# Optimization experiments

Hardware: AMD Instinct MI355X
Metric: run time of the kernel (lower is better)

## Reference

```python
import jax, jax.numpy as jnp
import numpy as np
from jax import lax

B, C, H, W = 8, 128, 256, 256
OUT_CH = 64
IN_CH = C * 9  # 1152: module's in_channels = 9 * image channels (unfold with 3x3 kernel)


def setup_inputs() -> dict:
    key = jax.random.key(0)
    k1, k2, k3 = jax.random.split(key, 3)
    x = jax.random.normal(k1, (B, C, H, W), dtype=jnp.float32)
    style = jax.random.normal(k2, (B, IN_CH), dtype=jnp.float32)
    # learned parameter: torch.randn(out_channels, in_channels, 1, 1) -> store as (out, in)
    weight = jax.random.normal(k3, (OUT_CH, IN_CH), dtype=jnp.float32)
    return {"x": x, "style": style, "weight": weight}


def reference(x, style, weight):
    b, c, h, w = x.shape
    out_ch, in_ch = weight.shape  # in_ch == c * 9
    # unfold column ordering is (c, kh, kw), so the flattened weight is exactly a
    # 3x3 conv kernel: (out, c*9) -> (out, c, 3, 3)
    w33 = weight.reshape(out_ch, c, 3, 3)
    # style.view(B,1,in_ch,1,1) * weight -> per-sample modulated 3x3 kernels
    w_mod = style.reshape(b, 1, c, 3, 3) * w33[None]  # (B, out, c, 3, 3)

    def conv_one(xi, wi):
        # xi: (c, h, w), wi: (out, c, 3, 3); SAME padding matches padding=(1,1)
        return lax.conv_general_dilated(
            xi[None], wi, window_strides=(1, 1), padding="SAME",
            dimension_numbers=("NCHW", "OIHW", "NCHW"))[0]

    out = jax.vmap(conv_one)(x, w_mod)  # (B, out, h, w)
    return out
```

## Files before the change

kernel.cpp:

```cpp
#include <hip/hip_runtime.h>
#include <hip/hip_bf16.h>

#define BATCH 8
#define CIN   128
#define HH    256
#define WW    256
#define OUTC  64
#define INCH  1152
#define HW    (HH*WW)

typedef __attribute__((ext_vector_type(8))) short short8;
typedef __attribute__((ext_vector_type(4))) float f32x4;

__device__ __forceinline__ unsigned short bf16r(float f) {
    unsigned u = __builtin_bit_cast(unsigned, f);
    u += 0x7fffu + ((u >> 16) & 1u);
    return (unsigned short)(u >> 16);
}

__global__ void __launch_bounds__(256) wmod_kernel(const float* __restrict__ weight,
                                                   const float* __restrict__ style,
                                                   unsigned short* __restrict__ wmod) {
    int i = blockIdx.x * 256 + threadIdx.x;
    if (i >= BATCH * 9 * OUTC * CIN) return;
    int c    = i & (CIN - 1);
    int rest = i >> 7;
    int o    = rest & (OUTC - 1);
    int bt   = rest >> 6;
    int tap  = bt % 9;
    int b    = bt / 9;
    int k    = c * 9 + tap;
    float v = weight[o * INCH + k] * style[b * INCH + k];
    wmod[i] = bf16r(v);
}

template <bool GW>
__global__ void __launch_bounds__(256, 4) conv_kernel(
    const float* __restrict__ x,
    const unsigned short* __restrict__ wmod,
    const float* __restrict__ weight,
    const float* __restrict__ style,
    float* __restrict__ out)
{
    __shared__ __align__(16) unsigned short xs_sm[170 * 64];

    const int tid = threadIdx.x;
    const int bx  = blockIdx.x;
    const int b   = blockIdx.y;
    const int h0  = (bx >> 3) * 8;
    const int w0  = (bx & 7) * 32;

    const int wv  = tid >> 6;
    const int l15 = tid & 15;
    const int kg  = (tid >> 4) & 3;

    int prow[4], pcol[4];
#pragma unroll
    for (int ni = 0; ni < 4; ++ni) {
        int p = wv * 64 + ni * 16 + l15;
        prow[ni] = p >> 5;
        pcol[ni] = p & 31;
    }

    f32x4 acc[4][4];
#pragma unroll
    for (int mi = 0; mi < 4; ++mi)
#pragma unroll
        for (int ni = 0; ni < 4; ++ni) acc[mi][ni] = (f32x4){0.f, 0.f, 0.f, 0.f};

    for (int chunk = 0; chunk < 4; ++chunk) {
        if (chunk) __syncthreads();

        const float* xb = x + ((size_t)(b * CIN + chunk * 32)) * HW;
        for (int t = tid; t < 1360; t += 256) {
            int cg  = t / 340;
            int s   = t - cg * 340;
            int r   = s / 34;
            int col = s - r * 34;
            int h = h0 - 1 + r, w = w0 - 1 + col;
            bool ok = ((unsigned)h < HH) && ((unsigned)w < WW);
            int off = h * WW + w;
            const float* xc = xb + (size_t)(cg * 8) * HW;
            short8 sv;
#pragma unroll
            for (int j = 0; j < 8; ++j) {
                float f = ok ? xc[(size_t)j * HW + off] : 0.f;
                sv[j] = (short)bf16r(f);
            }
            int q = s >> 1;
            int g = (((s & 1) << 2) | cg) ^ (q & 7);
            *(short8*)&xs_sm[q * 64 + g * 8] = sv;
        }
        __syncthreads();

        const unsigned short* wmb = wmod + ((size_t)(b * 9) * OUTC) * CIN + chunk * 32;
#pragma unroll
        for (int tap = 0; tap < 9; ++tap) {
            const int kh = tap / 3, kw = tap % 3;

            short8 A[4];
            if (GW) {
                const unsigned short* wt = wmb + (size_t)tap * OUTC * CIN;
#pragma unroll
                for (int mi = 0; mi < 4; ++mi)
                    A[mi] = *(const short8*)(wt + (mi * 16 + l15) * CIN + kg * 8);
            } else {
#pragma unroll
                for (int mi = 0; mi < 4; ++mi) {
                    int o = mi * 16 + l15;
#pragma unroll
                    for (int j = 0; j < 8; ++j) {
                        int c = chunk * 32 + kg * 8 + j;
                        int k = c * 9 + tap;
                        A[mi][j] = (short)bf16r(weight[o * INCH + k] *
                                                style[b * INCH + k]);
                    }
                }
            }

            short8 Bv[4];
#pragma unroll
            for (int ni = 0; ni < 4; ++ni) {
                int s = (prow[ni] + kh) * 34 + pcol[ni] + kw;
                int q = s >> 1;
                int g = (((s & 1) << 2) | kg) ^ (q & 7);
                Bv[ni] = *(const short8*)&xs_sm[q * 64 + g * 8];
            }
#pragma unroll
            for (int mi = 0; mi < 4; ++mi)
#pragma unroll
                for (int ni = 0; ni < 4; ++ni)
                    acc[mi][ni] = __builtin_amdgcn_mfma_f32_16x16x32_bf16(
                        A[mi], Bv[ni], acc[mi][ni], 0, 0, 0);
        }
    }

    float* op = out + ((size_t)b * OUTC) * HW;
#pragma unroll
    for (int mi = 0; mi < 4; ++mi) {
#pragma unroll
        for (int ni = 0; ni < 4; ++ni) {
            int p = wv * 64 + ni * 16 + l15;
            int h = h0 + (p >> 5), w = w0 + (p & 31);
#pragma unroll
            for (int r = 0; r < 4; ++r) {
                int o = mi * 16 + kg * 4 + r;
                op[(size_t)o * HW + h * WW + w] = acc[mi][ni][r];
            }
        }
    }
}

extern "C" void kernel_launch(void* const* d_in, const int* in_sizes, int n_in,
                              void* d_out, int out_size, void* d_ws, size_t ws_size,
                              hipStream_t stream) {
    const float* x      = (const float*)d_in[0];
    const float* style  = (const float*)d_in[1];
    const float* weight = (const float*)d_in[2];
    float* out = (float*)d_out;

    const size_t wmod_bytes = (size_t)BATCH * 9 * OUTC * CIN * sizeof(unsigned short);
    if (ws_size >= wmod_bytes) {
        int total = BATCH * 9 * OUTC * CIN;
        wmod_kernel<<<(total + 255) / 256, 256, 0, stream>>>(weight, style,
                                                             (unsigned short*)d_ws);
        conv_kernel<true><<<dim3(256, BATCH), 256, 0, stream>>>(
            x, (const unsigned short*)d_ws, nullptr, nullptr, out);
    } else {
        conv_kernel<false><<<dim3(256, BATCH), 256, 0, stream>>>(
            x, nullptr, weight, style, out);
    }
}
```

Measured before the change: 248.7 us.

## Double-buffer LDS input tiles to overlap staging with MFMA compute

Doubles the shared-memory input tile and restructures the channel-chunk loop so the next chunk is loaded and converted to bf16 while the current chunk runs its MFMAs, with one barrier per chunk instead of two. Per-thread staging offsets, bounds masks and swizzled LDS addresses are precomputed once rather than recomputed with divisions every chunk. The larger LDS footprint and extra registers lower the occupancy bound from 4 to 3 blocks per CU, which may reduce latency hiding elsewhere.

After: 306.7 us. 23.4% more time.

```diff
diff --git a/kernel.cpp b/kernel.cpp
--- a/kernel.cpp
+++ b/kernel.cpp
@@ -35,14 +35,14 @@
 }
 
 template <bool GW>
-__global__ void __launch_bounds__(256, 4) conv_kernel(
+__global__ void __launch_bounds__(256, 3) conv_kernel(
     const float* __restrict__ x,
     const unsigned short* __restrict__ wmod,
     const float* __restrict__ weight,
     const float* __restrict__ style,
     float* __restrict__ out)
 {
-    __shared__ __align__(16) unsigned short xs_sm[170 * 64];
+    __shared__ __align__(16) unsigned short xs_sm[2][170 * 64];
 
     const int tid = threadIdx.x;
     const int bx  = blockIdx.x;
@@ -54,6 +54,24 @@
     const int l15 = tid & 15;
     const int kg  = (tid >> 4) & 3;
 
+    int soff[6], slds[6];
+    unsigned sok = 0;
+#pragma unroll
+    for (int k = 0; k < 6; ++k) {
+        int t  = tid + k * 256;
+        int tt = (t < 1360) ? t : 0;
+        int cg  = tt / 340;
+        int s   = tt - cg * 340;
+        int r   = s / 34;
+        int col = s - r * 34;
+        int h = h0 - 1 + r, w = w0 - 1 + col;
+        if (((unsigned)h < HH) && ((unsigned)w < WW)) sok |= (1u << k);
+        soff[k] = cg * 8 * HW + h * WW + w;
+        int q = s >> 1;
+        int g = (((s & 1) << 2) | cg) ^ (q & 7);
+        slds[k] = q * 64 + g * 8;
+    }
+
     int prow[4], pcol[4];
 #pragma unroll
     for (int ni = 0; ni < 4; ++ni) {
@@ -68,32 +86,27 @@
 #pragma unroll
         for (int ni = 0; ni < 4; ++ni) acc[mi][ni] = (f32x4){0.f, 0.f, 0.f, 0.f};
 
-    for (int chunk = 0; chunk < 4; ++chunk) {
-        if (chunk) __syncthreads();
-
+    auto stage = [&](int chunk, unsigned short* xsb) {
         const float* xb = x + ((size_t)(b * CIN + chunk * 32)) * HW;
-        for (int t = tid; t < 1360; t += 256) {
-            int cg  = t / 340;
-            int s   = t - cg * 340;
-            int r   = s / 34;
-            int col = s - r * 34;
-            int h = h0 - 1 + r, w = w0 - 1 + col;
-            bool ok = ((unsigned)h < HH) && ((unsigned)w < WW);
-            int off = h * WW + w;
-            const float* xc = xb + (size_t)(cg * 8) * HW;
-            short8 sv;
-#pragma unroll
-            for (int j = 0; j < 8; ++j) {
-                float f = ok ? xc[(size_t)j * HW + off] : 0.f;
-                sv[j] = (short)bf16r(f);
-            }
-            int q = s >> 1;
-            int g = (((s & 1) << 2) | cg) ^ (q & 7);
-            *(short8*)&xs_sm[q * 64 + g * 8] = sv;
+#pragma unroll
+        for (int k = 0; k < 6; ++k) {
+            if (k < 5 || tid < 80) {
+                bool ok = (sok >> k) & 1u;
+                const float* xp = xb + soff[k];
+                short8 sv;
+#pragma unroll
+                for (int j = 0; j < 8; ++j) {
+                    float f = ok ? xp[(size_t)j * HW] : 0.f;
+                    sv[j] = (short)bf16r(f);
+                }
+                *(short8*)&xsb[slds[k]] = sv;
+            }
         }
-        __syncthreads();
-
-        const unsigned short* wmb = wmod + ((size_t)(b * 9) * OUTC) * CIN + chunk * 32;
+    };
+
+    auto compute = [&](int chunk, const unsigned short* xs) {
+        const unsigned short* wmb =
+            wmod + ((size_t)(b * 9) * OUTC) * CIN + chunk * 32;
 #pragma unroll
         for (int tap = 0; tap < 9; ++tap) {
             const int kh = tap / 3, kw = tap % 3;
@@ -124,7 +137,7 @@
                 int s = (prow[ni] + kh) * 34 + pcol[ni] + kw;
                 int q = s >> 1;
                 int g = (((s & 1) << 2) | kg) ^ (q & 7);
-                Bv[ni] = *(const short8*)&xs_sm[q * 64 + g * 8];
+                Bv[ni] = *(const short8*)&xs[q * 64 + g * 8];
             }
 #pragma unroll
             for (int mi = 0; mi < 4; ++mi)
@@ -133,7 +146,24 @@
                     acc[mi][ni] = __builtin_amdgcn_mfma_f32_16x16x32_bf16(
                         A[mi], Bv[ni], acc[mi][ni], 0, 0, 0);
         }
-    }
+    };
+
+    stage(0, xs_sm[0]);
+    __syncthreads();
+
+    stage(1, xs_sm[1]);
+    compute(0, xs_sm[0]);
+    __syncthreads();
+
+    stage(2, xs_sm[0]);
+    compute(1, xs_sm[1]);
+    __syncthreads();
+
+    stage(3, xs_sm[1]);
+    compute(2, xs_sm[0]);
+    __syncthreads();
+
+    compute(3, xs_sm[1]);
 
     float* op = out + ((size_t)b * OUTC) * HW;
 #pragma unroll
```

## Split output channels across 8 waves and vectorize halo tile loads

Applied to the files above, without the earlier changes.

The conv block grows from 4 to 8 waves: waves are arranged as 2 output-channel halves by 4 pixel groups, and each wave holds half as many accumulators. The shared-memory halo fill now uses 400 threads that each issue 16-byte float4 loads across 8 channels, with clamped addresses and masking, in place of scalar per-pixel loads. This is meant to raise latency hiding and occupancy and to cut global load instruction count. In exchange, each block reads the same B fragments from shared memory twice, and the launch bounds now ask for more waves per CU than the register budget may support.

Result: faster. 227.4 us (-8.5%).

```diff
diff --git a/kernel.cpp b/kernel.cpp
--- a/kernel.cpp
+++ b/kernel.cpp
@@ -35,7 +35,7 @@
 }
 
 template <bool GW>
-__global__ void __launch_bounds__(256, 4) conv_kernel(
+__global__ void __launch_bounds__(512, 4) conv_kernel(
     const float* __restrict__ x,
     const unsigned short* __restrict__ wmod,
     const float* __restrict__ weight,
@@ -51,45 +51,62 @@
     const int w0  = (bx & 7) * 32;
 
     const int wv  = tid >> 6;
+    const int wr  = wv >> 2;
+    const int wc  = wv & 3;
     const int l15 = tid & 15;
     const int kg  = (tid >> 4) & 3;
 
-    int prow[4], pcol[4];
+    int sbase[4];
 #pragma unroll
     for (int ni = 0; ni < 4; ++ni) {
-        int p = wv * 64 + ni * 16 + l15;
-        prow[ni] = p >> 5;
-        pcol[ni] = p & 31;
+        int p = wc * 64 + ni * 16 + l15;
+        sbase[ni] = (p >> 5) * 34 + (p & 31);
     }
 
-    f32x4 acc[4][4];
+    const bool tvalid = tid < 400;
+    const int scg = tvalid ? tid / 100 : 0;
+    const int srw = tvalid ? tid % 100 : 0;
+    const int sr  = srw / 10;
+    const int swq = srw % 10;
+    const int sh  = h0 - 1 + sr;
+    const bool hok = (unsigned)sh < HH;
+    const int wload  = w0 - 4 + swq * 4;
+    const int wclamp = min(max(wload, 0), WW - 4);
+    const int gbase  = (hok ? sh : 0) * WW + wclamp;
+
+    f32x4 acc[2][4];
 #pragma unroll
-    for (int mi = 0; mi < 4; ++mi)
+    for (int mi = 0; mi < 2; ++mi)
 #pragma unroll
         for (int ni = 0; ni < 4; ++ni) acc[mi][ni] = (f32x4){0.f, 0.f, 0.f, 0.f};
 
     for (int chunk = 0; chunk < 4; ++chunk) {
         if (chunk) __syncthreads();
 
-        const float* xb = x + ((size_t)(b * CIN + chunk * 32)) * HW;
-        for (int t = tid; t < 1360; t += 256) {
-            int cg  = t / 340;
-            int s   = t - cg * 340;
-            int r   = s / 34;
-            int col = s - r * 34;
-            int h = h0 - 1 + r, w = w0 - 1 + col;
-            bool ok = ((unsigned)h < HH) && ((unsigned)w < WW);
-            int off = h * WW + w;
-            const float* xc = xb + (size_t)(cg * 8) * HW;
-            short8 sv;
+        if (tvalid) {
+            const float* xp =
+                x + ((size_t)(b * CIN + chunk * 32 + scg * 8)) * HW + gbase;
+            f32x4 f[8];
 #pragma unroll
-            for (int j = 0; j < 8; ++j) {
-                float f = ok ? xc[(size_t)j * HW + off] : 0.f;
-                sv[j] = (short)bf16r(f);
+            for (int j = 0; j < 8; ++j)
+                f[j] = hok ? *(const f32x4*)(xp + (size_t)j * HW)
+                           : (f32x4){0.f, 0.f, 0.f, 0.f};
+#pragma unroll
+            for (int u = 0; u < 4; ++u) {
+                int w   = wload + u;
+                int col = w - (w0 - 1);
+                if (col >= 0 && col <= 33) {
+                    bool wok = hok && ((unsigned)w < WW);
+                    short8 sv;
+#pragma unroll
+                    for (int j = 0; j < 8; ++j)
+                        sv[j] = wok ? (short)bf16r(f[j][u]) : (short)0;
+                    int s = sr * 34 + col;
+                    int q = s >> 1;
+                    int g = (((s & 1) << 2) | scg) ^ (q & 7);
+                    *(short8*)&xs_sm[q * 64 + g * 8] = sv;
+                }
             }
-            int q = s >> 1;
-            int g = (((s & 1) << 2) | cg) ^ (q & 7);
-            *(short8*)&xs_sm[q * 64 + g * 8] = sv;
         }
         __syncthreads();
 
@@ -98,16 +115,17 @@
         for (int tap = 0; tap < 9; ++tap) {
             const int kh = tap / 3, kw = tap % 3;
 
-            short8 A[4];
+            short8 A[2];
             if (GW) {
                 const unsigned short* wt = wmb + (size_t)tap * OUTC * CIN;
 #pragma unroll
-                for (int mi = 0; mi < 4; ++mi)
-                    A[mi] = *(const short8*)(wt + (mi * 16 + l15) * CIN + kg * 8);
+                for (int mi = 0; mi < 2; ++mi)
+                    A[mi] = *(const short8*)(wt + (wr * 32 + mi * 16 + l15) * CIN +
+                                             kg * 8);
             } else {
 #pragma unroll
-                for (int mi = 0; mi < 4; ++mi) {
-                    int o = mi * 16 + l15;
+                for (int mi = 0; mi < 2; ++mi) {
+                    int o = wr * 32 + mi * 16 + l15;
 #pragma unroll
                     for (int j = 0; j < 8; ++j) {
                         int c = chunk * 32 + kg * 8 + j;
@@ -121,13 +139,13 @@
             short8 Bv[4];
 #pragma unroll
             for (int ni = 0; ni < 4; ++ni) {
-                int s = (prow[ni] + kh) * 34 + pcol[ni] + kw;
+                int s = sbase[ni] + kh * 34 + kw;
                 int q = s >> 1;
                 int g = (((s & 1) << 2) | kg) ^ (q & 7);
                 Bv[ni] = *(const short8*)&xs_sm[q * 64 + g * 8];
             }
 #pragma unroll
-            for (int mi = 0; mi < 4; ++mi)
+            for (int mi = 0; mi < 2; ++mi)
 #pragma unroll
                 for (int ni = 0; ni < 4; ++ni)
                     acc[mi][ni] = __builtin_amdgcn_mfma_f32_16x16x32_bf16(
@@ -137,14 +155,14 @@
 
     float* op = out + ((size_t)b * OUTC) * HW;
 #pragma unroll
-    for (int mi = 0; mi < 4; ++mi) {
+    for (int mi = 0; mi < 2; ++mi) {
 #pragma unroll
         for (int ni = 0; ni < 4; ++ni) {
-            int p = wv * 64 + ni * 16 + l15;
+            int p = wc * 64 + ni * 16 + l15;
             int h = h0 + (p >> 5), w = w0 + (p & 31);
 #pragma unroll
             for (int r = 0; r < 4; ++r) {
-                int o = mi * 16 + kg * 4 + r;
+                int o = wr * 32 + mi * 16 + kg * 4 + r;
                 op[(size_t)o * HW + h * WW + w] = acc[mi][ni][r];
             }
         }
@@ -164,10 +182,10 @@
         int total = BATCH * 9 * OUTC * CIN;
         wmod_kernel<<<(total + 255) / 256, 256, 0, stream>>>(weight, style,
                                                              (unsigned short*)d_ws);
-        conv_kernel<true><<<dim3(256, BATCH), 256, 0, stream>>>(
+        conv_kernel<true><<<dim3(256, BATCH), 512, 0, stream>>>(
             x, (const unsigned short*)d_ws, nullptr, nullptr, out);
     } else {
-        conv_kernel<false><<<dim3(256, BATCH), 256, 0, stream>>>(
+        conv_kernel<false><<<dim3(256, BATCH), 512, 0, stream>>>(
             x, nullptr, weight, style, out);
     }
 }
```
